# Kernel optimization log

Hardware: AMD Instinct MI355X
Metric: run time of the kernel (lower is better)

## Reference

```python
import jax, jax.numpy as jnp
import numpy as np

NUM_HEADS = 32
KV_HEADS = 8
HEAD_DIM = 64
HIDDEN = 2048
ROPE_THETA = 10000.0


def setup_inputs() -> dict:
    key = jax.random.key(0)
    ks = jax.random.split(key, 5)
    B, S, H = 2, 2048, HIDDEN
    scale = 0.02
    return {
        "x": jax.random.normal(ks[0], (B, S, H), dtype=jnp.float32),
        # weights stored as (in_features, out_features)
        "Wq": jax.random.normal(ks[1], (H, NUM_HEADS * HEAD_DIM), dtype=jnp.float32) * scale,
        "Wk": jax.random.normal(ks[2], (H, KV_HEADS * HEAD_DIM), dtype=jnp.float32) * scale,
        "Wv": jax.random.normal(ks[3], (H, KV_HEADS * HEAD_DIM), dtype=jnp.float32) * scale,
        "Wo": jax.random.normal(ks[4], (H, H), dtype=jnp.float32) * scale,
    }


def _rope_tables(seq_len, dtype):
    # freq over even dims, angles concatenated twice -> (S, HEAD_DIM)
    freq = 1.0 / (ROPE_THETA ** (jnp.arange(0, HEAD_DIM, 2, dtype=jnp.float32) / HEAD_DIM))
    ang = jnp.arange(seq_len, dtype=jnp.float32)[:, None] * freq[None, :]
    emb = jnp.concatenate([ang, ang], axis=-1)
    return jnp.cos(emb).astype(dtype), jnp.sin(emb).astype(dtype)


def _rotate_half(x):
    x1, x2 = jnp.split(x, 2, axis=-1)
    return jnp.concatenate([-x2, x1], axis=-1)


def reference(x, Wq, Wk, Wv, Wo):
    B, S, H = x.shape
    q = jnp.einsum("bsd,df->bsf", x, Wq).reshape(B, S, NUM_HEADS, HEAD_DIM).transpose(0, 2, 1, 3)
    k = jnp.einsum("bsd,df->bsf", x, Wk).reshape(B, S, KV_HEADS, HEAD_DIM).transpose(0, 2, 1, 3)
    v = jnp.einsum("bsd,df->bsf", x, Wv).reshape(B, S, KV_HEADS, HEAD_DIM).transpose(0, 2, 1, 3)

    cos, sin = _rope_tables(S, x.dtype)  # (S, HEAD_DIM), broadcasts over (B, h, S, D)
    q = q * cos + _rotate_half(q) * sin
    k = k * cos + _rotate_half(k) * sin

    n_rep = NUM_HEADS // KV_HEADS
    k = jnp.repeat(k, n_rep, axis=1)  # (B, NUM_HEADS, S, D)
    v = jnp.repeat(v, n_rep, axis=1)

    scores = jnp.einsum("bhsd,bhtd->bhst", q, k) / jnp.sqrt(jnp.asarray(HEAD_DIM, x.dtype))
    weights = jax.nn.softmax(scores, axis=-1)
    ctx = jnp.einsum("bhst,bhtd->bhsd", weights, v)
    ctx = ctx.transpose(0, 2, 1, 3).reshape(B, S, H)
    return jnp.einsum("bsd,df->bsf", ctx, Wo)
```

## Files before the change

### kernel.cpp

```cpp
#include <hip/hip_runtime.h>

typedef short s8v __attribute__((ext_vector_type(8)));
typedef int i2v __attribute__((ext_vector_type(2)));
typedef float f2v __attribute__((ext_vector_type(2)));
typedef float f4v __attribute__((ext_vector_type(4)));

typedef const __attribute__((address_space(1))) char* gp1_t;
typedef __attribute__((address_space(3))) char* lp3_t;

__device__ __forceinline__ float bf2f(short s) {
    union { unsigned u; float f; } c;
    c.u = ((unsigned)(unsigned short)s) << 16;
    return c.f;
}
__device__ __forceinline__ short f2bf(float f) {
    union { float f; unsigned u; } c; c.f = f;
    unsigned r = (c.u + 0x7FFFu + ((c.u >> 16) & 1u)) >> 16;
    return (short)r;
}
__device__ __forceinline__ unsigned cvt_pk_bf16(float a, float b) {
    unsigned r;
    asm("v_cvt_pk_bf16_f32 %0, %1, %2" : "=v"(r) : "v"(a), "v"(b));
    return r;
}
__device__ __forceinline__ s8v cvt8(const float* __restrict__ p) {
    f4v a = *(const f4v*)p;
    f4v b = *(const f4v*)(p + 4);
    s8v r;
    r[0] = f2bf(a[0]); r[1] = f2bf(a[1]); r[2] = f2bf(a[2]); r[3] = f2bf(a[3]);
    r[4] = f2bf(b[0]); r[5] = f2bf(b[1]); r[6] = f2bf(b[2]); r[7] = f2bf(b[3]);
    return r;
}


__global__ __launch_bounds__(256) void cvt_x(const float* __restrict__ x,
                                             short* __restrict__ xb) {
    long i = ((long)blockIdx.x * 256 + threadIdx.x) * 8;
    *(s8v*)&xb[i] = cvt8(&x[i]);
}

__global__ __launch_bounds__(256) void cvt_wt(const float* __restrict__ W,
                                              short* __restrict__ Wt,
                                              int N, int obase, float scale) {
    __shared__ __align__(16) short tile[64 * 72];
    const int kt = blockIdx.y * 64, n0 = blockIdx.x * 64;
    const int t = threadIdx.x;
    const int r = t >> 4, c4 = (t & 15) * 4;
#pragma unroll
    for (int i = 0; i < 4; i++) {
        int kr = r + i * 16;
        f4v v = *(const f4v*)&W[(long)(kt + kr) * N + n0 + c4];
#pragma unroll
        for (int j = 0; j < 4; j++) tile[(c4 + j) * 72 + kr] = f2bf(v[j] * scale);
    }
    __syncthreads();
    const int nr = t >> 3, kc = (t & 7) * 8;
#pragma unroll
    for (int i = 0; i < 2; i++) {
        int n = nr + i * 32;
        *(s8v*)&Wt[(long)(obase + n0 + n) * 2048 + kt + kc] = *(const s8v*)&tile[n * 72 + kc];
    }
}

template <bool CF32>
__global__ __launch_bounds__(512, 2) void gemm_bt8(const short* __restrict__ A,
                                                   const short* __restrict__ Bt,
                                                   void* __restrict__ Cv,
                                                   int K, int lda, int ldb, int ldc) {
    __shared__ __align__(16) short Ab[2][16384];
    __shared__ __align__(16) short Bb[2][16384];

    const int tid = threadIdx.x;
    const int lane = tid & 63;
    const int wave = tid >> 6;
    const int quad = lane >> 4;
    const int l15 = lane & 15;

    const int nwg = gridDim.x * gridDim.y;
    int f = blockIdx.y * gridDim.x + blockIdx.x;
    if ((nwg & 7) == 0) f = (f & 7) * (nwg >> 3) + (f >> 3);
    const int m0 = (f / gridDim.x) * 256;
    const int n0 = (f % gridDim.x) * 256;

    const int wm = (wave >> 2) * 128;
    const int wn = (wave & 3) * 64;

    const int rsub = lane >> 3;
    const int sslot = (lane & 7) ^ rsub;
    const short* aS[2][2];
    const short* bS[2][2];
#pragma unroll
    for (int h = 0; h < 2; h++)
#pragma unroll
        for (int i = 0; i < 2; i++) {
            int row = h * 128 + wave * 16 + i * 8 + rsub;
            aS[h][i] = A  + (long)(m0 + row) * lda + sslot * 8;
            bS[h][i] = Bt + (long)(n0 + row) * ldb + sslot * 8;
        }

    auto stageA = [&](int buf, int h, int kt) {
        char* d = (char*)&Ab[buf][0] + h * 16384 + wave * 2048;
        __builtin_amdgcn_global_load_lds((gp1_t)(aS[h][0] + (long)kt * 64), (lp3_t)d, 16, 0, 0);
        __builtin_amdgcn_global_load_lds((gp1_t)(aS[h][1] + (long)kt * 64), (lp3_t)(d + 1024), 16, 0, 0);
    };
    auto stageB = [&](int buf, int h, int kt) {
        char* d = (char*)&Bb[buf][0] + h * 16384 + wave * 2048;
        __builtin_amdgcn_global_load_lds((gp1_t)(bS[h][0] + (long)kt * 64), (lp3_t)d, 16, 0, 0);
        __builtin_amdgcn_global_load_lds((gp1_t)(bS[h][1] + (long)kt * 64), (lp3_t)(d + 1024), 16, 0, 0);
    };

    const int ks0 = (quad ^ (l15 & 7)) * 8;
    const int ks1 = ks0 ^ 32;

    f4v acc[2][4][2][2];
#pragma unroll
    for (int a = 0; a < 2; a++)
#pragma unroll
        for (int b = 0; b < 4; b++)
#pragma unroll
            for (int c = 0; c < 2; c++)
#pragma unroll
                for (int d = 0; d < 2; d++) acc[a][b][c][d] = (f4v){0.f, 0.f, 0.f, 0.f};

    const int NT = K >> 6;

    stageB(0, 0, 0); stageB(0, 1, 0); stageA(0, 0, 0); stageA(0, 1, 0);
    stageB(1, 0, 1); stageB(1, 1, 1); stageA(1, 0, 1);
    asm volatile("s_waitcnt vmcnt(6)" ::: "memory");
    __builtin_amdgcn_s_barrier();

    for (int t = 0; t < NT; ++t) {
        const short* Ac = &Ab[t & 1][0];
        const short* Bc = &Bb[t & 1][0];
        const int nb = (t + 1) & 1;
        s8v af[4][2], bf0[2][2], bf1[2][2];

#pragma unroll
        for (int mi = 0; mi < 4; mi++) {
            const int row = wm + mi * 16 + l15;
            af[mi][0] = *(const s8v*)&Ac[row * 64 + ks0];
            af[mi][1] = *(const s8v*)&Ac[row * 64 + ks1];
        }
#pragma unroll
        for (int ni = 0; ni < 2; ni++) {
            const int row = wn + ni * 16 + l15;
            bf0[ni][0] = *(const s8v*)&Bc[row * 64 + ks0];
            bf0[ni][1] = *(const s8v*)&Bc[row * 64 + ks1];
        }
        if (t + 1 < NT) stageA(nb, 1, t + 1);
        __builtin_amdgcn_s_setprio(1);
#pragma unroll
        for (int mi = 0; mi < 4; mi++)
#pragma unroll
            for (int ni = 0; ni < 2; ni++) {
                acc[0][mi][0][ni] = __builtin_amdgcn_mfma_f32_16x16x32_bf16(af[mi][0], bf0[ni][0], acc[0][mi][0][ni], 0, 0, 0);
                acc[0][mi][0][ni] = __builtin_amdgcn_mfma_f32_16x16x32_bf16(af[mi][1], bf0[ni][1], acc[0][mi][0][ni], 0, 0, 0);
            }
        __builtin_amdgcn_s_setprio(0);
        __builtin_amdgcn_s_barrier();

#pragma unroll
        for (int ni = 0; ni < 2; ni++) {
            const int row = wn + 32 + ni * 16 + l15;
            bf1[ni][0] = *(const s8v*)&Bc[row * 64 + ks0];
            bf1[ni][1] = *(const s8v*)&Bc[row * 64 + ks1];
        }
        __builtin_amdgcn_s_setprio(1);
#pragma unroll
        for (int mi = 0; mi < 4; mi++)
#pragma unroll
            for (int ni = 0; ni < 2; ni++) {
                acc[0][mi][1][ni] = __builtin_amdgcn_mfma_f32_16x16x32_bf16(af[mi][0], bf1[ni][0], acc[0][mi][1][ni], 0, 0, 0);
                acc[0][mi][1][ni] = __builtin_amdgcn_mfma_f32_16x16x32_bf16(af[mi][1], bf1[ni][1], acc[0][mi][1][ni], 0, 0, 0);
            }
        __builtin_amdgcn_s_setprio(0);
        __builtin_amdgcn_s_barrier();

#pragma unroll
        for (int mi = 0; mi < 4; mi++) {
            const int row = wm + 64 + mi * 16 + l15;
            af[mi][0] = *(const s8v*)&Ac[row * 64 + ks0];
            af[mi][1] = *(const s8v*)&Ac[row * 64 + ks1];
        }
        if (t + 2 < NT) stageB(t & 1, 0, t + 2);
        __builtin_amdgcn_s_setprio(1);
#pragma unroll
        for (int mi = 0; mi < 4; mi++)
#pragma unroll
            for (int ni = 0; ni < 2; ni++) {
                acc[1][mi][0][ni] = __builtin_amdgcn_mfma_f32_16x16x32_bf16(af[mi][0], bf0[ni][0], acc[1][mi][0][ni], 0, 0, 0);
                acc[1][mi][0][ni] = __builtin_amdgcn_mfma_f32_16x16x32_bf16(af[mi][1], bf0[ni][1], acc[1][mi][0][ni], 0, 0, 0);
            }
        __builtin_amdgcn_s_setprio(0);
        __builtin_amdgcn_s_barrier();

        if (t + 2 < NT) { stageB(t & 1, 1, t + 2); stageA(t & 1, 0, t + 2); }
        __builtin_amdgcn_s_setprio(1);
#pragma unroll
        for (int mi = 0; mi < 4; mi++)
#pragma unroll
            for (int ni = 0; ni < 2; ni++) {
                acc[1][mi][1][ni] = __builtin_amdgcn_mfma_f32_16x16x32_bf16(af[mi][0], bf1[ni][0], acc[1][mi][1][ni], 0, 0, 0);
                acc[1][mi][1][ni] = __builtin_amdgcn_mfma_f32_16x16x32_bf16(af[mi][1], bf1[ni][1], acc[1][mi][1][ni], 0, 0, 0);
            }
        __builtin_amdgcn_s_setprio(0);
        if (t + 1 < NT) {
            if (t + 1 == NT - 1) asm volatile("s_waitcnt vmcnt(0)" ::: "memory");
            else                 asm volatile("s_waitcnt vmcnt(6)" ::: "memory");
            __builtin_amdgcn_s_barrier();
        }
    }

#pragma unroll
    for (int qm = 0; qm < 2; qm++)
#pragma unroll
        for (int mi = 0; mi < 4; mi++)
#pragma unroll
            for (int qn = 0; qn < 2; qn++)
#pragma unroll
                for (int ni = 0; ni < 2; ni++)
#pragma unroll
                    for (int r = 0; r < 4; r++) {
                        int row = m0 + wm + qm * 64 + mi * 16 + quad * 4 + r;
                        int col = n0 + wn + qn * 32 + ni * 16 + l15;
                        float v = acc[qm][mi][qn][ni][r];
                        if (CF32) ((float*)Cv)[(long)row * ldc + col] = v;
                        else      ((short*)Cv)[(long)row * ldc + col] = f2bf(v);
                    }
}

__global__ __launch_bounds__(256) void rope_kernel(short* __restrict__ qkv) {
    int tid = blockIdx.x * 256 + threadIdx.x;
    int p = tid % 1280;
    int row = tid / 1280;
    int head = p >> 5;
    int j = p & 31;
    int s = row & 2047;
    int c1 = head * 64 + j;
    float freq = exp2f(-(float)j * 0.4152410118609203f);
    float ang = (float)s * freq;
    float sn, cs;
    __sincosf(ang, &sn, &cs);
    long base = (long)row * 3072;
    float x1 = bf2f(qkv[base + c1]);
    float x2 = bf2f(qkv[base + c1 + 32]);
    qkv[base + c1]      = f2bf(x1 * cs - x2 * sn);
    qkv[base + c1 + 32] = f2bf(x2 * cs + x1 * sn);
}

__global__ __launch_bounds__(256) void vtrans(const short* __restrict__ qkv,
                                              short* __restrict__ Vt_g) {
    __shared__ __align__(16) short tile[64 * 72];
    const int kt = blockIdx.x * 64;
    const int kvh = blockIdx.y;
    const int b = blockIdx.z;
    const int t = threadIdx.x;
#pragma unroll
    for (int cc = 0; cc < 2; cc++) {
        int ch = t + cc * 256;
        int key = ch >> 3, d0 = (ch & 7) * 8;
        s8v v = *(const s8v*)&qkv[(long)(b * 2048 + kt + key) * 3072 + 2560 + kvh * 64 + d0];
#pragma unroll
        for (int i = 0; i < 8; i++) tile[(d0 + i) * 72 + key] = v[i];
    }
    __syncthreads();
#pragma unroll
    for (int cc = 0; cc < 2; cc++) {
        int ch = t + cc * 256;
        int d = ch >> 3, kc = (ch & 7) * 8;
        *(s8v*)&Vt_g[(long)((b * 8 + kvh) * 64 + d) * 2048 + kt + kc] = *(const s8v*)&tile[d * 72 + kc];
    }
}

__global__ __launch_bounds__(256, 3) void attn4(short* __restrict__ qkv,
                                                const short* __restrict__ Vt_g) {
    __shared__ __align__(16) short KV[2][2][4096];
    __shared__ __align__(16) short Ps[4][2][16 * 72];
    __shared__ float rsb[4][32];

    const int tid = threadIdx.x;
    const int lane = tid & 63;
    const int wave = tid >> 6;
    const int quad = lane >> 4;
    const int l15 = lane & 15;

    int f = (blockIdx.z * 32 + blockIdx.y) * 16 + blockIdx.x;
    f = (f & 7) * 128 + (f >> 3);
    const int b = f >> 9;
    const int h = (f >> 4) & 31;
    const int kvh = h >> 2;
    const int q0 = (f & 15) * 128;

    const long kbase = ((long)b * 2048) * 3072 + 2048 + kvh * 64;
    const long vtbase = (long)(b * 8 + kvh) * 64 * 2048;

    const long qrow = (long)b * 2048 + q0 + wave * 32 + l15;
    const short* qp = qkv + qrow * 3072 + h * 64 + quad * 8;
    const s8v qf00 = *(const s8v*)(qp);
    const s8v qf01 = *(const s8v*)(qp + 32);
    const s8v qf10 = *(const s8v*)(qp + 16 * 3072);
    const s8v qf11 = *(const s8v*)(qp + 16 * 3072 + 32);

    const int rA = wave * 8 + (lane >> 3);
    const int sslot = (lane & 7) ^ (lane >> 3);
    const short* kA = qkv + kbase + (long)rA * 3072 + sslot * 8;
    const short* kB = kA + (long)32 * 3072;
    const short* vA = Vt_g + vtbase + (long)rA * 2048 + sslot * 8;
    const short* vB = vA + (long)32 * 2048;

    {
        char* kd = (char*)&KV[0][0][0] + wave * 1024;
        char* vd = (char*)&KV[0][1][0] + wave * 1024;
        __builtin_amdgcn_global_load_lds((gp1_t)kA, (lp3_t)kd, 16, 0, 0);
        __builtin_amdgcn_global_load_lds((gp1_t)kB, (lp3_t)(kd + 4096), 16, 0, 0);
        __builtin_amdgcn_global_load_lds((gp1_t)vA, (lp3_t)vd, 16, 0, 0);
        __builtin_amdgcn_global_load_lds((gp1_t)vB, (lp3_t)(vd + 4096), 16, 0, 0);
    }
    __syncthreads();

    const int ks0 = ((quad ^ (l15 & 7)) << 3);
    const int ks1 = ks0 ^ 32;

    f2v rs0v = (f2v){0.f, 0.f}, rs1v = (f2v){0.f, 0.f};
    f4v o0[4], o1[4];
#pragma unroll
    for (int ni = 0; ni < 4; ni++) { o0[ni] = (f4v){0.f, 0.f, 0.f, 0.f}; o1[ni] = (f4v){0.f, 0.f, 0.f, 0.f}; }

    short* Pw0 = &Ps[wave][0][0];
    short* Pw1 = &Ps[wave][1][0];

    for (int t = 0; t < 32; ++t) {
        const short* Kb = &KV[t & 1][0][0];
        const short* Vb = &KV[t & 1][1][0];

        if (t < 31) {
            const long ko = (long)(t + 1) * (64 * 3072);
            const long vo = (long)(t + 1) * 64;
            char* kd = (char*)&KV[(t + 1) & 1][0][0] + wave * 1024;
            char* vd = (char*)&KV[(t + 1) & 1][1][0] + wave * 1024;
            __builtin_amdgcn_global_load_lds((gp1_t)(kA + ko), (lp3_t)kd, 16, 0, 0);
            __builtin_amdgcn_global_load_lds((gp1_t)(kB + ko), (lp3_t)(kd + 4096), 16, 0, 0);
            __builtin_amdgcn_global_load_lds((gp1_t)(vA + vo), (lp3_t)vd, 16, 0, 0);
            __builtin_amdgcn_global_load_lds((gp1_t)(vB + vo), (lp3_t)(vd + 4096), 16, 0, 0);
        }

#pragma unroll
        for (int ni = 0; ni < 4; ni++) {
            const int ro = (ni * 16 + l15) * 64;
            const s8v kf0 = *(const s8v*)&Kb[ro + ks0];
            const s8v kf1 = *(const s8v*)&Kb[ro + ks1];
            f4v a = (f4v){-24.f, -24.f, -24.f, -24.f};
            a = __builtin_amdgcn_mfma_f32_16x16x32_bf16(kf0, qf00, a, 0, 0, 0);
            a = __builtin_amdgcn_mfma_f32_16x16x32_bf16(kf1, qf01, a, 0, 0, 0);
            {
                float p0 = exp2f(a[0]);
                float p1 = exp2f(a[1]);
                float p2 = exp2f(a[2]);
                float p3 = exp2f(a[3]);
                rs0v += (f2v){p0, p1};
                rs0v += (f2v){p2, p3};
                *(i2v*)&Pw0[l15 * 72 + ni * 16 + quad * 4] =
                    (i2v){(int)cvt_pk_bf16(p0, p1), (int)cvt_pk_bf16(p2, p3)};
            }
            f4v c = (f4v){-24.f, -24.f, -24.f, -24.f};
            c = __builtin_amdgcn_mfma_f32_16x16x32_bf16(kf0, qf10, c, 0, 0, 0);
            c = __builtin_amdgcn_mfma_f32_16x16x32_bf16(kf1, qf11, c, 0, 0, 0);
            {
                float p0 = exp2f(c[0]);
                float p1 = exp2f(c[1]);
                float p2 = exp2f(c[2]);
                float p3 = exp2f(c[3]);
                rs1v += (f2v){p0, p1};
                rs1v += (f2v){p2, p3};
                *(i2v*)&Pw1[l15 * 72 + ni * 16 + quad * 4] =
                    (i2v){(int)cvt_pk_bf16(p0, p1), (int)cvt_pk_bf16(p2, p3)};
            }
        }

        const s8v pf00 = *(const s8v*)&Pw0[l15 * 72 + quad * 8];
        const s8v pf01 = *(const s8v*)&Pw0[l15 * 72 + 32 + quad * 8];
        const s8v pf10 = *(const s8v*)&Pw1[l15 * 72 + quad * 8];
        const s8v pf11 = *(const s8v*)&Pw1[l15 * 72 + 32 + quad * 8];
#pragma unroll
        for (int ni = 0; ni < 4; ni++) {
            const int ro = (ni * 16 + l15) * 64;
            const s8v vf0 = *(const s8v*)&Vb[ro + ks0];
            const s8v vf1 = *(const s8v*)&Vb[ro + ks1];
            o0[ni] = __builtin_amdgcn_mfma_f32_16x16x32_bf16(pf00, vf0, o0[ni], 0, 0, 0);
            o0[ni] = __builtin_amdgcn_mfma_f32_16x16x32_bf16(pf01, vf1, o0[ni], 0, 0, 0);
            o1[ni] = __builtin_amdgcn_mfma_f32_16x16x32_bf16(pf10, vf0, o1[ni], 0, 0, 0);
            o1[ni] = __builtin_amdgcn_mfma_f32_16x16x32_bf16(pf11, vf1, o1[ni], 0, 0, 0);
        }
        __syncthreads();
    }

    float rs0 = rs0v[0] + rs0v[1];
    float rs1 = rs1v[0] + rs1v[1];
    rs0 += __shfl_xor(rs0, 16); rs0 += __shfl_xor(rs0, 32);
    rs1 += __shfl_xor(rs1, 16); rs1 += __shfl_xor(rs1, 32);
    if (quad == 0) { rsb[wave][l15] = rs0; rsb[wave][16 + l15] = rs1; }
    __syncthreads();

#pragma unroll
    for (int r = 0; r < 4; r++) {
        const float i0 = 1.0f / rsb[wave][quad * 4 + r];
        const float i1 = 1.0f / rsb[wave][16 + quad * 4 + r];
        const long ob0 = ((long)b * 2048 + q0 + wave * 32 + quad * 4 + r) * 3072 + h * 64;
        const long ob1 = ob0 + 16 * 3072;
#pragma unroll
        for (int ni = 0; ni < 4; ni++) {
            qkv[ob0 + ni * 16 + l15] = f2bf(o0[ni][r] * i0);
            qkv[ob1 + ni * 16 + l15] = f2bf(o1[ni][r] * i1);
        }
    }
}


template <bool AF32, bool CF32>
__global__ __launch_bounds__(256) void gemm_bn(const void* __restrict__ Av,
                                               const float* __restrict__ B,
                                               void* __restrict__ Cv,
                                               int K, int N, int lda, int ldc) {
    __shared__ __align__(16) short As[128 * 40];
    __shared__ __align__(16) short Bs[128 * 40];
    const int tid = threadIdx.x;
    const int lane = tid & 63;
    const int wave = tid >> 6;
    const int quad = lane >> 4;
    const int l15 = lane & 15;
    const int m0 = blockIdx.y * 128;
    const int n0 = blockIdx.x * 128;
    const int wm = (wave & 1) * 64;
    const int wn = (wave >> 1) * 64;

    f4v acc[4][4];
#pragma unroll
    for (int i = 0; i < 4; i++)
#pragma unroll
        for (int j = 0; j < 4; j++) acc[i][j] = (f4v){0.f, 0.f, 0.f, 0.f};

    const int ar0 = tid >> 2, akc0 = (tid & 3) * 8;
    const int ar1 = (tid + 256) >> 2, akc1 = ((tid + 256) & 3) * 8;
    const int bk0 = tid >> 4, bnc0 = (tid & 15) * 8;
    const int bk1 = (tid + 256) >> 4, bnc1 = ((tid + 256) & 15) * 8;

    for (int k0 = 0; k0 < K; k0 += 32) {
        __syncthreads();
        if (AF32) {
            const float* A = (const float*)Av;
            *(s8v*)(&As[ar0 * 40 + akc0]) = cvt8(&A[(long)(m0 + ar0) * lda + k0 + akc0]);
            *(s8v*)(&As[ar1 * 40 + akc1]) = cvt8(&A[(long)(m0 + ar1) * lda + k0 + akc1]);
        } else {
            const short* A = (const short*)Av;
            *(s8v*)(&As[ar0 * 40 + akc0]) = *(const s8v*)(&A[(long)(m0 + ar0) * lda + k0 + akc0]);
            *(s8v*)(&As[ar1 * 40 + akc1]) = *(const s8v*)(&A[(long)(m0 + ar1) * lda + k0 + akc1]);
        }
        s8v b0 = cvt8(&B[(long)(k0 + bk0) * N + n0 + bnc0]);
        s8v b1 = cvt8(&B[(long)(k0 + bk1) * N + n0 + bnc1]);
#pragma unroll
        for (int i = 0; i < 8; i++) Bs[(bnc0 + i) * 40 + bk0] = b0[i];
#pragma unroll
        for (int i = 0; i < 8; i++) Bs[(bnc1 + i) * 40 + bk1] = b1[i];
        __syncthreads();
        s8v af[4], bfr[4];
#pragma unroll
        for (int mi = 0; mi < 4; mi++)
            af[mi] = *(const s8v*)(&As[(wm + mi * 16 + l15) * 40 + quad * 8]);
#pragma unroll
        for (int ni = 0; ni < 4; ni++)
            bfr[ni] = *(const s8v*)(&Bs[(wn + ni * 16 + l15) * 40 + quad * 8]);
#pragma unroll
        for (int mi = 0; mi < 4; mi++)
#pragma unroll
            for (int ni = 0; ni < 4; ni++)
                acc[mi][ni] = __builtin_amdgcn_mfma_f32_16x16x32_bf16(af[mi], bfr[ni], acc[mi][ni], 0, 0, 0);
    }
#pragma unroll
    for (int mi = 0; mi < 4; mi++)
#pragma unroll
        for (int ni = 0; ni < 4; ni++)
#pragma unroll
            for (int r = 0; r < 4; r++) {
                int row = m0 + wm + mi * 16 + quad * 4 + r;
                int col = n0 + wn + ni * 16 + l15;
                if (CF32) ((float*)Cv)[(long)row * ldc + col] = acc[mi][ni][r];
                else      ((short*)Cv)[(long)row * ldc + col] = f2bf(acc[mi][ni][r]);
            }
}

__global__ __launch_bounds__(256) void attn_kernel(short* __restrict__ qkv) {
    __shared__ __align__(16) short Qs[64 * 72];
    __shared__ __align__(16) short Ks[64 * 72];
    __shared__ __align__(16) short Vt[64 * 72];
    __shared__ __align__(16) short Ps[4][16 * 72];

    const int tid = threadIdx.x;
    const int lane = tid & 63;
    const int wave = tid >> 6;
    const int quad = lane >> 4;
    const int l15 = lane & 15;
    const int b = blockIdx.z;
    const int h = blockIdx.y;
    const int kvh = h >> 2;
    const int q0 = blockIdx.x * 64;

    const long qbase = ((long)b * 2048 + q0) * 3072 + h * 64;
    const long kbase = ((long)b * 2048) * 3072 + 2048 + kvh * 64;
    const long vbase = kbase + 512;

#pragma unroll
    for (int cc = 0; cc < 2; cc++) {
        int ch = tid + cc * 256;
        int r = ch >> 3, d0 = (ch & 7) * 8;
        *(s8v*)(&Qs[r * 72 + d0]) = *(const s8v*)(&qkv[qbase + (long)r * 3072 + d0]);
    }
    __syncthreads();
    s8v qf[2];
    qf[0] = *(const s8v*)(&Qs[(wave * 16 + l15) * 72 + quad * 8]);
    qf[1] = *(const s8v*)(&Qs[(wave * 16 + l15) * 72 + 32 + quad * 8]);

    float m_i[4], l_i[4];
    f4v o[4];
#pragma unroll
    for (int r = 0; r < 4; r++) { m_i[r] = -1e30f; l_i[r] = 0.0f; }
#pragma unroll
    for (int ni = 0; ni < 4; ni++) o[ni] = (f4v){0.f, 0.f, 0.f, 0.f};

    for (int kt = 0; kt < 2048; kt += 64) {
        __syncthreads();
#pragma unroll
        for (int cc = 0; cc < 2; cc++) {
            int ch = tid + cc * 256;
            int r = ch >> 3, d0 = (ch & 7) * 8;
            *(s8v*)(&Ks[r * 72 + d0]) = *(const s8v*)(&qkv[kbase + (long)(kt + r) * 3072 + d0]);
            s8v v = *(const s8v*)(&qkv[vbase + (long)(kt + r) * 3072 + d0]);
            int g = d0 >> 3;
            int chn = ((r >> 3) ^ g) * 8 + (r & 7);
#pragma unroll
            for (int i = 0; i < 8; i++) Vt[(d0 + i) * 72 + chn] = v[i];
        }
        __syncthreads();

        f4v sc[4];
#pragma unroll
        for (int ni = 0; ni < 4; ni++) {
            s8v kf0 = *(const s8v*)(&Ks[(ni * 16 + l15) * 72 + quad * 8]);
            s8v kf1 = *(const s8v*)(&Ks[(ni * 16 + l15) * 72 + 32 + quad * 8]);
            f4v a = (f4v){0.f, 0.f, 0.f, 0.f};
            a = __builtin_amdgcn_mfma_f32_16x16x32_bf16(qf[0], kf0, a, 0, 0, 0);
            a = __builtin_amdgcn_mfma_f32_16x16x32_bf16(qf[1], kf1, a, 0, 0, 0);
            sc[ni] = a * 0.125f;
        }
        float alpha[4], rs[4];
#pragma unroll
        for (int r = 0; r < 4; r++) {
            float v = fmaxf(fmaxf(sc[0][r], sc[1][r]), fmaxf(sc[2][r], sc[3][r]));
            v = fmaxf(v, __shfl_xor(v, 1));
            v = fmaxf(v, __shfl_xor(v, 2));
            v = fmaxf(v, __shfl_xor(v, 4));
            v = fmaxf(v, __shfl_xor(v, 8));
            float mn = fmaxf(m_i[r], v);
            alpha[r] = __expf(m_i[r] - mn);
            m_i[r] = mn;
            rs[r] = 0.f;
        }
#pragma unroll
        for (int ni = 0; ni < 4; ni++)
#pragma unroll
            for (int r = 0; r < 4; r++) {
                float pv = __expf(sc[ni][r] - m_i[r]);
                sc[ni][r] = pv;
                rs[r] += pv;
            }
#pragma unroll
        for (int r = 0; r < 4; r++) {
            float v = rs[r];
            v += __shfl_xor(v, 1);
            v += __shfl_xor(v, 2);
            v += __shfl_xor(v, 4);
            v += __shfl_xor(v, 8);
            l_i[r] = l_i[r] * alpha[r] + v;
        }
#pragma unroll
        for (int ni = 0; ni < 4; ni++)
#pragma unroll
            for (int r = 0; r < 4; r++) {
                int row = quad * 4 + r;
                int key = ni * 16 + l15;
                int chn = ((key >> 3) ^ (row >> 3)) * 8 + (key & 7);
                Ps[wave][row * 72 + chn] = f2bf(sc[ni][r]);
            }
        __syncthreads();
#pragma unroll
        for (int ni = 0; ni < 4; ni++) {
            f4v t = o[ni];
            t[0] *= alpha[0]; t[1] *= alpha[1]; t[2] *= alpha[2]; t[3] *= alpha[3];
            o[ni] = t;
        }
        s8v pf0 = *(const s8v*)(&Ps[wave][l15 * 72 + ((quad ^ (l15 >> 3)) * 8)]);
        s8v pf1 = *(const s8v*)(&Ps[wave][l15 * 72 + (((4 + quad) ^ (l15 >> 3)) * 8)]);
#pragma unroll
        for (int ni = 0; ni < 4; ni++) {
            int d = ni * 16 + l15;
            s8v vf0 = *(const s8v*)(&Vt[d * 72 + ((quad ^ (d >> 3)) * 8)]);
            s8v vf1 = *(const s8v*)(&Vt[d * 72 + (((4 + quad) ^ (d >> 3)) * 8)]);
            o[ni] = __builtin_amdgcn_mfma_f32_16x16x32_bf16(pf0, vf0, o[ni], 0, 0, 0);
            o[ni] = __builtin_amdgcn_mfma_f32_16x16x32_bf16(pf1, vf1, o[ni], 0, 0, 0);
        }
    }
#pragma unroll
    for (int r = 0; r < 4; r++) {
        float inv = 1.0f / l_i[r];
        int srow = q0 + wave * 16 + quad * 4 + r;
        long obase = ((long)b * 2048 + srow) * 3072 + h * 64;
#pragma unroll
        for (int ni = 0; ni < 4; ni++)
            qkv[obase + ni * 16 + l15] = f2bf(o[ni][r] * inv);
    }
}

extern "C" void kernel_launch(void* const* d_in, const int* in_sizes, int n_in,
                              void* d_out, int out_size, void* d_ws, size_t ws_size,
                              hipStream_t stream) {
    (void)in_sizes; (void)n_in; (void)out_size;
    const float* x  = (const float*)d_in[0];
    const float* Wq = (const float*)d_in[1];
    const float* Wk = (const float*)d_in[2];
    const float* Wv = (const float*)d_in[3];
    const float* Wo = (const float*)d_in[4];

    const float CS = 0.18033688011112042f;
    const size_t need = 67108864ULL;
    if (ws_size >= need) {
        short* xb    = (short*)d_ws;
        short* Wqkvt = xb + 8388608;
        short* Wot   = Wqkvt + 6291456;
        short* qkv   = Wot + 4194304;
        short* Vt_g  = qkv + 12582912;

        cvt_x<<<4096, 256, 0, stream>>>(x, xb);
        cvt_wt<<<dim3(32, 32), 256, 0, stream>>>(Wq, Wqkvt, 2048, 0, 1.0f);
        cvt_wt<<<dim3(8, 32), 256, 0, stream>>>(Wk, Wqkvt, 512, 2048, CS);
        cvt_wt<<<dim3(8, 32), 256, 0, stream>>>(Wv, Wqkvt, 512, 2560, 1.0f);
        cvt_wt<<<dim3(32, 32), 256, 0, stream>>>(Wo, Wot, 2048, 0, 1.0f);
        gemm_bt8<false><<<dim3(12, 16), 512, 0, stream>>>(xb, Wqkvt, qkv, 2048, 2048, 2048, 3072);
        rope_kernel<<<dim3(20480), 256, 0, stream>>>(qkv);
        vtrans<<<dim3(32, 8, 2), 256, 0, stream>>>(qkv, Vt_g);
        attn4<<<dim3(16, 32, 2), 256, 0, stream>>>(qkv, Vt_g);
        gemm_bt8<true><<<dim3(8, 16), 512, 0, stream>>>(qkv, Wot, d_out, 2048, 3072, 2048, 2048);
    } else {
        short* qkv = (short*)d_ws;
        gemm_bn<true, false><<<dim3(16, 32), 256, 0, stream>>>(x, Wq, qkv,        2048, 2048, 2048, 3072);
        gemm_bn<true, false><<<dim3(4, 32), 256, 0, stream>>>(x, Wk, qkv + 2048, 2048,  512, 2048, 3072);
        gemm_bn<true, false><<<dim3(4, 32), 256, 0, stream>>>(x, Wv, qkv + 2560, 2048,  512, 2048, 3072);
        rope_kernel<<<dim3(20480), 256, 0, stream>>>(qkv);
        attn_kernel<<<dim3(32, 32, 2), 256, 0, stream>>>(qkv);
        gemm_bn<false, true><<<dim3(16, 32), 256, 0, stream>>>(qkv, Wo, d_out, 2048, 2048, 3072, 2048);
    }
}
```

Measured before the change: 357.3 us.

## Fuse RoPE into QKV GEMM epilogue and use 128-row tiles for output projection

RoPE is now applied to the QKV GEMM accumulators in registers before they are stored, which removes the separate rope kernel launch and its read-modify-write pass over Q and K. The output projection switches to a new GEMM variant with 128x256 tiles, doubling the grid from 128 to 256 workgroups so the MI355X's compute units are better occupied. The fused rotation adds sincos work to the GEMM epilogue. It relies on each wave's column layout pairing the first and second 32 dims of a head.

```diff
diff --git a/kernel.cpp b/kernel.cpp
--- a/kernel.cpp
+++ b/kernel.cpp
@@ -62,7 +62,7 @@
     }
 }
 
-template <bool CF32>
+template <bool CF32, bool ROPE>
 __global__ __launch_bounds__(512, 2) void gemm_bt8(const short* __restrict__ A,
                                                    const short* __restrict__ Bt,
                                                    void* __restrict__ Cv,
@@ -211,6 +211,29 @@
         }
     }
 
+    if (ROPE && (n0 + wn) < 2560) {
+        const float NLOG = -0.4152410118609203f;
+        const float fr0 = exp2f((float)l15 * NLOG);
+        const float fr1 = exp2f((float)(16 + l15) * NLOG);
+#pragma unroll
+        for (int qm = 0; qm < 2; qm++)
+#pragma unroll
+            for (int mi = 0; mi < 4; mi++)
+#pragma unroll
+                for (int r = 0; r < 4; r++) {
+                    const float s = (float)((m0 + wm + qm * 64 + mi * 16 + quad * 4 + r) & 2047);
+#pragma unroll
+                    for (int ni = 0; ni < 2; ni++) {
+                        float sn, cs;
+                        __sincosf(s * (ni ? fr1 : fr0), &sn, &cs);
+                        float x1 = acc[qm][mi][0][ni][r];
+                        float x2 = acc[qm][mi][1][ni][r];
+                        acc[qm][mi][0][ni][r] = x1 * cs - x2 * sn;
+                        acc[qm][mi][1][ni][r] = x2 * cs + x1 * sn;
+                    }
+                }
+    }
+
 #pragma unroll
     for (int qm = 0; qm < 2; qm++)
 #pragma unroll
@@ -227,6 +250,166 @@
                         if (CF32) ((float*)Cv)[(long)row * ldc + col] = v;
                         else      ((short*)Cv)[(long)row * ldc + col] = f2bf(v);
                     }
+}
+
+template <bool CF32>
+__global__ __launch_bounds__(512, 2) void gemm_bt2(const short* __restrict__ A,
+                                                   const short* __restrict__ Bt,
+                                                   void* __restrict__ Cv,
+                                                   int K, int lda, int ldb, int ldc) {
+    __shared__ __align__(16) short Ab[2][8192];
+    __shared__ __align__(16) short Bb[2][16384];
+
+    const int tid = threadIdx.x;
+    const int lane = tid & 63;
+    const int wave = tid >> 6;
+    const int quad = lane >> 4;
+    const int l15 = lane & 15;
+
+    const int nwg = gridDim.x * gridDim.y;
+    int f = blockIdx.y * gridDim.x + blockIdx.x;
+    if ((nwg & 7) == 0) f = (f & 7) * (nwg >> 3) + (f >> 3);
+    const int m0 = (f / gridDim.x) * 128;
+    const int n0 = (f % gridDim.x) * 256;
+
+    const int wm = (wave >> 2) * 64;
+    const int wn = (wave & 3) * 64;
+
+    const int rsub = lane >> 3;
+    const int sslot = (lane & 7) ^ rsub;
+    const short* aS[2];
+    const short* bS[4];
+#pragma unroll
+    for (int i = 0; i < 2; i++)
+        aS[i] = A + (long)(m0 + wave * 16 + i * 8 + rsub) * lda + sslot * 8;
+#pragma unroll
+    for (int i = 0; i < 4; i++)
+        bS[i] = Bt + (long)(n0 + wave * 32 + i * 8 + rsub) * ldb + sslot * 8;
+
+    auto stageA = [&](int buf, int kt) {
+        char* d = (char*)&Ab[buf][0] + wave * 2048;
+        __builtin_amdgcn_global_load_lds((gp1_t)(aS[0] + (long)kt * 64), (lp3_t)d, 16, 0, 0);
+        __builtin_amdgcn_global_load_lds((gp1_t)(aS[1] + (long)kt * 64), (lp3_t)(d + 1024), 16, 0, 0);
+    };
+    auto stageBh = [&](int buf, int h, int kt) {
+        char* d = (char*)&Bb[buf][0] + wave * 4096 + h * 2048;
+        __builtin_amdgcn_global_load_lds((gp1_t)(bS[2 * h] + (long)kt * 64), (lp3_t)d, 16, 0, 0);
+        __builtin_amdgcn_global_load_lds((gp1_t)(bS[2 * h + 1] + (long)kt * 64), (lp3_t)(d + 1024), 16, 0, 0);
+    };
+
+    const int ks0 = (quad ^ (l15 & 7)) * 8;
+    const int ks1 = ks0 ^ 32;
+
+    f4v acc[4][2][2];
+#pragma unroll
+    for (int a = 0; a < 4; a++)
+#pragma unroll
+        for (int b = 0; b < 2; b++)
+#pragma unroll
+            for (int c = 0; c < 2; c++) acc[a][b][c] = (f4v){0.f, 0.f, 0.f, 0.f};
+
+    const int NT = K >> 6;
+
+    stageA(0, 0); stageBh(0, 0, 0); stageBh(0, 1, 0);
+    stageA(1, 1); stageBh(1, 0, 1); stageBh(1, 1, 1);
+    asm volatile("s_waitcnt vmcnt(6)" ::: "memory");
+    __builtin_amdgcn_s_barrier();
+
+    for (int t = 0; t < NT; ++t) {
+        const short* Ac = &Ab[t & 1][0];
+        const short* Bc = &Bb[t & 1][0];
+        s8v af01[2][2], af23[2][2], bf0[2][2], bf1[2][2];
+
+#pragma unroll
+        for (int mi = 0; mi < 2; mi++) {
+            const int row = wm + mi * 16 + l15;
+            af01[mi][0] = *(const s8v*)&Ac[row * 64 + ks0];
+            af01[mi][1] = *(const s8v*)&Ac[row * 64 + ks1];
+        }
+#pragma unroll
+        for (int ni = 0; ni < 2; ni++) {
+            const int row = wn + ni * 16 + l15;
+            bf0[ni][0] = *(const s8v*)&Bc[row * 64 + ks0];
+            bf0[ni][1] = *(const s8v*)&Bc[row * 64 + ks1];
+        }
+        __builtin_amdgcn_s_setprio(1);
+#pragma unroll
+        for (int mi = 0; mi < 2; mi++)
+#pragma unroll
+            for (int ni = 0; ni < 2; ni++) {
+                acc[mi][0][ni] = __builtin_amdgcn_mfma_f32_16x16x32_bf16(af01[mi][0], bf0[ni][0], acc[mi][0][ni], 0, 0, 0);
+                acc[mi][0][ni] = __builtin_amdgcn_mfma_f32_16x16x32_bf16(af01[mi][1], bf0[ni][1], acc[mi][0][ni], 0, 0, 0);
+            }
+        __builtin_amdgcn_s_setprio(0);
+        __builtin_amdgcn_s_barrier();
+
+#pragma unroll
+        for (int ni = 0; ni < 2; ni++) {
+            const int row = wn + 32 + ni * 16 + l15;
+            bf1[ni][0] = *(const s8v*)&Bc[row * 64 + ks0];
+            bf1[ni][1] = *(const s8v*)&Bc[row * 64 + ks1];
+        }
+        if (t + 2 < NT) stageBh(t & 1, 0, t + 2);
+        __builtin_amdgcn_s_setprio(1);
+#pragma unroll
+        for (int mi = 0; mi < 2; mi++)
+#pragma unroll
+            for (int ni = 0; ni < 2; ni++) {
+                acc[mi][1][ni] = __builtin_amdgcn_mfma_f32_16x16x32_bf16(af01[mi][0], bf1[ni][0], acc[mi][1][ni], 0, 0, 0);
+                acc[mi][1][ni] = __builtin_amdgcn_mfma_f32_16x16x32_bf16(af01[mi][1], bf1[ni][1], acc[mi][1][ni], 0, 0, 0);
+            }
+        __builtin_amdgcn_s_setprio(0);
+        __builtin_amdgcn_s_barrier();
+
+#pragma unroll
+        for (int mi = 0; mi < 2; mi++) {
+            const int row = wm + 32 + mi * 16 + l15;
+            af23[mi][0] = *(const s8v*)&Ac[row * 64 + ks0];
+            af23[mi][1] = *(const s8v*)&Ac[row * 64 + ks1];
+        }
+        if (t + 2 < NT) stageBh(t & 1, 1, t + 2);
+        __builtin_amdgcn_s_setprio(1);
+#pragma unroll
+        for (int mi = 0; mi < 2; mi++)
+#pragma unroll
+            for (int ni = 0; ni < 2; ni++) {
+                acc[2 + mi][0][ni] = __builtin_amdgcn_mfma_f32_16x16x32_bf16(af23[mi][0], bf0[ni][0], acc[2 + mi][0][ni], 0, 0, 0);
+                acc[2 + mi][0][ni] = __builtin_amdgcn_mfma_f32_16x16x32_bf16(af23[mi][1], bf0[ni][1], acc[2 + mi][0][ni], 0, 0, 0);
+            }
+        __builtin_amdgcn_s_setprio(0);
+        __builtin_amdgcn_s_barrier();
+
+        if (t + 2 < NT) stageA(t & 1, t + 2);
+        __builtin_amdgcn_s_setprio(1);
+#pragma unroll
+        for (int mi = 0; mi < 2; mi++)
+#pragma unroll
+            for (int ni = 0; ni < 2; ni++) {
+                acc[2 + mi][1][ni] = __builtin_amdgcn_mfma_f32_16x16x32_bf16(af23[mi][0], bf1[ni][0], acc[2 + mi][1][ni], 0, 0, 0);
+                acc[2 + mi][1][ni] = __builtin_amdgcn_mfma_f32_16x16x32_bf16(af23[mi][1], bf1[ni][1], acc[2 + mi][1][ni], 0, 0, 0);
+            }
+        __builtin_amdgcn_s_setprio(0);
+        if (t + 1 < NT) {
+            if (t + 1 == NT - 1) asm volatile("s_waitcnt vmcnt(0)" ::: "memory");
+            else                 asm volatile("s_waitcnt vmcnt(6)" ::: "memory");
+            __builtin_amdgcn_s_barrier();
+        }
+    }
+
+#pragma unroll
+    for (int mi = 0; mi < 4; mi++)
+#pragma unroll
+        for (int qn = 0; qn < 2; qn++)
+#pragma unroll
+            for (int ni = 0; ni < 2; ni++)
+#pragma unroll
+                for (int r = 0; r < 4; r++) {
+                    int row = m0 + wm + mi * 16 + quad * 4 + r;
+                    int col = n0 + wn + qn * 32 + ni * 16 + l15;
+                    float v = acc[mi][qn][ni][r];
+                    if (CF32) ((float*)Cv)[(long)row * ldc + col] = v;
+                    else      ((short*)Cv)[(long)row * ldc + col] = f2bf(v);
+                }
 }
 
 __global__ __launch_bounds__(256) void rope_kernel(short* __restrict__ qkv) {
@@ -643,11 +826,10 @@
         cvt_wt<<<dim3(8, 32), 256, 0, stream>>>(Wk, Wqkvt, 512, 2048, CS);
         cvt_wt<<<dim3(8, 32), 256, 0, stream>>>(Wv, Wqkvt, 512, 2560, 1.0f);
         cvt_wt<<<dim3(32, 32), 256, 0, stream>>>(Wo, Wot, 2048, 0, 1.0f);
-        gemm_bt8<false><<<dim3(12, 16), 512, 0, stream>>>(xb, Wqkvt, qkv, 2048, 2048, 2048, 3072);
-        rope_kernel<<<dim3(20480), 256, 0, stream>>>(qkv);
+        gemm_bt8<false, true><<<dim3(12, 16), 512, 0, stream>>>(xb, Wqkvt, qkv, 2048, 2048, 2048, 3072);
         vtrans<<<dim3(32, 8, 2), 256, 0, stream>>>(qkv, Vt_g);
         attn4<<<dim3(16, 32, 2), 256, 0, stream>>>(qkv, Vt_g);
-        gemm_bt8<true><<<dim3(8, 16), 512, 0, stream>>>(qkv, Wot, d_out, 2048, 3072, 2048, 2048);
+        gemm_bt2<true><<<dim3(8, 32), 512, 0, stream>>>(qkv, Wot, d_out, 2048, 3072, 2048, 2048);
     } else {
         short* qkv = (short*)d_ws;
         gemm_bn<true, false><<<dim3(16, 32), 256, 0, stream>>>(x, Wq, qkv,        2048, 2048, 2048, 3072);
```

Result: faster. 333.5 us (-6.7%).
